# Kernel optimization log

Hardware: AMD Instinct MI355X
Metric: run time of the kernel (lower is better)

The kernel has to match this reference:

```python
import jax, jax.numpy as jnp
import numpy as np

DY = jnp.array([-1, -1, -1, 0, 0, 0, 1, 1, 1], dtype=jnp.float32)
DX = jnp.array([-1, 0, 1, -1, 0, 1, -1, 0, 1], dtype=jnp.float32)
REG = jnp.stack([DY, DX])  # (2,9) regular_matrix: row0 = dy, row1 = dx
EPS = 1e-5


def conv3x3(x, w, b):
    y = jax.lax.conv_general_dilated(x, w, (1, 1), ((1, 1), (1, 1)),
                                     dimension_numbers=('NCHW', 'OIHW', 'NCHW'))
    return y + b[None, :, None, None]


def batchnorm(x, gamma, beta):
    m = x.mean((0, 2, 3), keepdims=True)
    v = x.var((0, 2, 3), keepdims=True)
    return gamma[None, :, None, None] * (x - m) * jax.lax.rsqrt(v + EPS) + beta[None, :, None, None]


def make_offset(tm, tr):
    # tm: (N,4,H,W) per-pixel 2x2 matrix, tr: (N,2,H,W) translation
    N, _, H, W = tm.shape
    M = tm.transpose(0, 2, 3, 1).reshape(N, H, W, 2, 2)
    off = jnp.einsum('nhwij,jk->nhwik', M, REG) - REG          # (N,H,W,2,9)
    off = off.transpose(0, 4, 3, 1, 2)                          # (N,9,2,H,W)
    off = off + tr[:, None, :, :, :]                            # broadcast translation over K
    return off


def deform_conv(x, off, w):
    # x: (N,C,H,W), off: (N,9,2,H,W) with [...,0]=dy,[...,1]=dx, w: (Co,C,3,3)
    N, C, H, W = x.shape
    K = 9
    py = jnp.arange(H, dtype=x.dtype)[None, None, :, None] + DY[None, :, None, None] + off[:, :, 0]
    px = jnp.arange(W, dtype=x.dtype)[None, None, None, :] + DX[None, :, None, None] + off[:, :, 1]
    y0 = jnp.floor(py)
    x0 = jnp.floor(px)
    wy = py - y0
    wx = px - x0
    y0i = y0.astype(jnp.int32)
    x0i = x0.astype(jnp.int32)
    x_flat = x.reshape(N, C, H * W)

    def corner(yi, xi, wgt):
        valid = (yi >= 0) & (yi < H) & (xi >= 0) & (xi < W)
        idx = jnp.clip(yi, 0, H - 1) * W + jnp.clip(xi, 0, W - 1)   # (N,K,H,W)
        g = jax.vmap(lambda xf, ix: xf[:, ix])(x_flat, idx.reshape(N, -1))
        g = g.reshape(N, C, K, H, W)
        return g * (wgt * valid)[:, None]

    cols = (corner(y0i, x0i, (1 - wy) * (1 - wx))
            + corner(y0i, x0i + 1, (1 - wy) * wx)
            + corner(y0i + 1, x0i, wy * (1 - wx))
            + corner(y0i + 1, x0i + 1, wy * wx))
    Co = w.shape[0]
    return jnp.einsum('nckhw,ock->nohw', cols, w.reshape(Co, C, K))


def setup_inputs() -> dict:
    key = jax.random.key(0)
    ks = jax.random.split(key, 16)
    N, C, Co, H, W = 4, 256, 256, 64, 64
    s_off = 0.02   # small init so offsets stay near the regular grid
    s_w = 0.05
    return {
        'x': jax.random.normal(ks[0], (N, C, H, W), jnp.float32),
        'tm1_w': jax.random.normal(ks[1], (4, C, 3, 3), jnp.float32) * s_off,
        'tm1_b': jax.random.normal(ks[2], (4,), jnp.float32) * s_off,
        'tr1_w': jax.random.normal(ks[3], (2, C, 3, 3), jnp.float32) * s_off,
        'tr1_b': jax.random.normal(ks[4], (2,), jnp.float32) * s_off,
        'dcn1_w': jax.random.normal(ks[5], (Co, C, 3, 3), jnp.float32) * s_w,
        'bn1_g': jnp.ones((Co,), jnp.float32),
        'bn1_b': jnp.zeros((Co,), jnp.float32),
        'tm2_w': jax.random.normal(ks[6], (4, Co, 3, 3), jnp.float32) * s_off,
        'tm2_b': jax.random.normal(ks[7], (4,), jnp.float32) * s_off,
        'tr2_w': jax.random.normal(ks[8], (2, Co, 3, 3), jnp.float32) * s_off,
        'tr2_b': jax.random.normal(ks[9], (2,), jnp.float32) * s_off,
        'dcn2_w': jax.random.normal(ks[10], (Co, Co, 3, 3), jnp.float32) * s_w,
        'bn2_g': jnp.ones((Co,), jnp.float32),
        'bn2_b': jnp.zeros((Co,), jnp.float32),
    }


def reference(x, tm1_w, tm1_b, tr1_w, tr1_b, dcn1_w, bn1_g, bn1_b,
              tm2_w, tm2_b, tr2_w, tr2_b, dcn2_w, bn2_g, bn2_b):
    residual = x
    off1 = make_offset(conv3x3(x, tm1_w, tm1_b), conv3x3(x, tr1_w, tr1_b))
    out = deform_conv(x, off1, dcn1_w)
    out = jax.nn.relu(batchnorm(out, bn1_g, bn1_b))
    off2 = make_offset(conv3x3(out, tm2_w, tm2_b), conv3x3(out, tr2_w, tr2_b))
    out = deform_conv(out, off2, dcn2_w)
    out = batchnorm(out, bn2_g, bn2_b)
    return jax.nn.relu(out + residual)
```

## Files before the change

kernel.cpp:

```cpp
#include <hip/hip_runtime.h>
#include <hip/hip_bf16.h>

#define HH 64
#define WW 64
#define HWSZ 4096
#define NBATCH 4
#define CCH 256
#define NPIX 16384
#define CK 2304
#define KSPLIT 3
#define EPSB 1e-5f

typedef __attribute__((ext_vector_type(8))) short bf16x8;
typedef __attribute__((ext_vector_type(4))) float f32x4;

static __device__ __forceinline__ unsigned short f2bf(float f){
  __hip_bfloat16 h = __float2bfloat16(f);
  return *(unsigned short*)&h;
}

__global__ __launch_bounds__(256) void k_transpose_in(const float* __restrict__ x,
                                                      float* __restrict__ xT){
  __shared__ float tile[64][65];
  int hw0 = blockIdx.x * 64;
  int c0  = blockIdx.y * 64;
  int n   = blockIdx.z;
  int t = threadIdx.x;
  int col = t & 63, rb = t >> 6;
#pragma unroll
  for (int r = 0; r < 16; ++r){
    int cl = rb + r*4;
    tile[cl][col] = x[(size_t)(n*CCH + c0 + cl)*HWSZ + hw0 + col];
  }
  __syncthreads();
#pragma unroll
  for (int r = 0; r < 16; ++r){
    int hwl = rb + r*4;
    xT[(size_t)(n*HWSZ + hw0 + hwl)*CCH + c0 + col] = tile[col][hwl];
  }
}

__global__ void k_woff_perm(const float* __restrict__ tmw, const float* __restrict__ trw,
                            float* __restrict__ woff){
  int idx = blockIdx.x*256 + threadIdx.x;
  if (idx >= 9*6*CCH) return;
  int k = idx / (6*CCH); int rem = idx % (6*CCH); int j = rem >> 8; int c = rem & 255;
  float v = (j < 4) ? tmw[(size_t)(j*CCH + c)*9 + k]
                    : trw[(size_t)((j-4)*CCH + c)*9 + k];
  woff[idx] = v;
}

__global__ void k_wgemm_perm(const float* __restrict__ w, __hip_bfloat16* __restrict__ wp){
  int idx = blockIdx.x*256 + threadIdx.x;
  if (idx >= CCH*CK) return;
  int blk = idx >> 13;
  int e   = idx & 8191;
  int o   = e >> 5;
  int el  = e & 31;
  int tap = blk >> 3, cb = blk & 7;
  int c   = cb*32 + (el ^ ((o & 3) << 3));
  wp[idx] = __float2bfloat16(w[(size_t)o*CK + c*9 + tap]);
}

__global__ __launch_bounds__(256) void k_offsets(const float* __restrict__ src,
    const float* __restrict__ wofft, const float* __restrict__ tmb,
    const float* __restrict__ trb, float* __restrict__ off){
  int t = threadIdx.x;
  int wid = t >> 6, lane = t & 63;
  int pbase = blockIdx.x*32 + wid*8;
  int n = pbase >> 12; int hw = pbase & 4095; int h = hw >> 6; int w0 = hw & 63;
  const float* base = src + (size_t)n*HWSZ*CCH + lane*4;

  float acc[8][6];
#pragma unroll
  for (int pi = 0; pi < 8; ++pi)
#pragma unroll
    for (int j = 0; j < 6; ++j) acc[pi][j] = 0.f;

  for (int k = 0; k < 9; ++k){
    int ky = k/3 - 1, kx = k%3 - 1;
    int yy = h + ky;
    if (yy < 0 || yy >= HH) continue;
    float4 wv[6];
#pragma unroll
    for (int j = 0; j < 6; ++j)
      wv[j] = *(const float4*)(wofft + ((k*6 + j) << 8) + lane*4);
#pragma unroll
    for (int pi = 0; pi < 8; ++pi){
      int xx = w0 + pi + kx;
      if (xx < 0 || xx >= WW) continue;
      float4 s4 = *(const float4*)(base + (size_t)(yy*WW + xx)*CCH);
#pragma unroll
      for (int j = 0; j < 6; ++j)
        acc[pi][j] += s4.x*wv[j].x + s4.y*wv[j].y + s4.z*wv[j].z + s4.w*wv[j].w;
    }
  }

#pragma unroll
  for (int pi = 0; pi < 8; ++pi)
#pragma unroll
    for (int j = 0; j < 6; ++j){
      float v = acc[pi][j];
#pragma unroll
      for (int m = 32; m >= 1; m >>= 1) v += __shfl_xor(v, m);
      acc[pi][j] = v;
    }

  float b0 = tmb[0], b1 = tmb[1], b2 = tmb[2], b3 = tmb[3];
  float c0 = trb[0], c1 = trb[1];
  if (lane < 18){
    int k = lane >> 1, comp = lane & 1;
    float dy = (float)(k/3 - 1), dx = (float)(k%3 - 1);
#pragma unroll
    for (int pi = 0; pi < 8; ++pi){
      int p = pbase + pi;
      float val;
      if (comp == 0)
        val = (acc[pi][0] + b0)*dy + (acc[pi][1] + b1)*dx - dy + acc[pi][4] + c0;
      else
        val = (acc[pi][2] + b2)*dy + (acc[pi][3] + b3)*dx - dx + acc[pi][5] + c1;
      off[((size_t)p*9 + k)*2 + comp] = val;
    }
  }
}

__global__ __launch_bounds__(512) void k_dcn(const float* __restrict__ src,
    const float* __restrict__ off, const __hip_bfloat16* __restrict__ wp,
    float* __restrict__ P){
  __shared__ __hip_bfloat16 Al[64*32];
  __shared__ __hip_bfloat16 Bl[256*32];
  __shared__ __align__(16) int   t_off[192][4];
  __shared__ __align__(16) float t_w[192][4];

  int t = threadIdx.x;
  int z = blockIdx.y;
  int pbase = blockIdx.x * 64;

  if (t < 192){
    int px = t / 3, ti = t - px*3;
    int k = z*3 + ti;
    int p = pbase + px;
    int n = p >> 12; int hw = p & 4095; int h = hw >> 6; int w = hw & 63;
    float2 of = *(const float2*)(off + ((size_t)p*9 + k)*2);
    float py = (float)(h + k/3 - 1) + of.x;
    float px_ = (float)(w + (k - (k/3)*3) - 1) + of.y;
    float y0f = floorf(py), x0f = floorf(px_);
    float wy = py - y0f, wx = px_ - x0f;
    int y0 = (int)y0f, x0 = (int)x0f;
    int y1 = y0 + 1, x1 = x0 + 1;
    float w00 = (1.f-wy)*(1.f-wx), w01 = (1.f-wy)*wx;
    float w10 = wy*(1.f-wx),       w11 = wy*wx;
    if (y0 < 0 || y0 >= HH) { w00 = 0.f; w01 = 0.f; }
    if (y1 < 0 || y1 >= HH) { w10 = 0.f; w11 = 0.f; }
    if (x0 < 0 || x0 >= WW) { w00 = 0.f; w10 = 0.f; }
    if (x1 < 0 || x1 >= WW) { w01 = 0.f; w11 = 0.f; }
    int y0c = min(max(y0,0),HH-1), y1c = min(max(y1,0),HH-1);
    int x0c = min(max(x0,0),WW-1), x1c = min(max(x1,0),WW-1);
    int pbix = n << 12;
    t_off[t][0] = (pbix + y0c*WW + x0c) << 10;
    t_off[t][1] = (pbix + y0c*WW + x1c) << 10;
    t_off[t][2] = (pbix + y1c*WW + x0c) << 10;
    t_off[t][3] = (pbix + y1c*WW + x1c) << 10;
    t_w[t][0] = w00; t_w[t][1] = w01; t_w[t][2] = w10; t_w[t][3] = w11;
  }
  __syncthreads();

  int wid = t >> 6, lane = t & 63;
  int pxl = t >> 3, q = t & 7;
  int px3 = pxl * 3, qb = q * 16;
  const char* sbase = (const char*)src;

  int abyte = pxl*64 + ((q*8) ^ ((pxl & 3) << 4));

  int kq = lane >> 4, fr = lane & 15;
  int abr[4], bbr[2];
#pragma unroll
  for (int mi = 0; mi < 4; ++mi){
    int apx = mi*16 + fr;
    abr[mi] = apx*64 + ((kq*16) ^ ((apx & 3) << 4));
  }
#pragma unroll
  for (int ni = 0; ni < 2; ++ni){
    int o = wid*32 + ni*16 + fr;
    bbr[ni] = o*64 + ((kq*16) ^ ((o & 3) << 4));
  }

  f32x4 acc[4][2];
#pragma unroll
  for (int i = 0; i < 4; ++i)
#pragma unroll
    for (int j = 0; j < 2; ++j)
      acc[i][j] = (f32x4){0.f,0.f,0.f,0.f};

  float4 ga, gb, gc, gd, wv;
  {
    int4 o4 = *(const int4*)t_off[px3];
    wv = *(const float4*)t_w[px3];
    ga = *(const float4*)(sbase + (size_t)(unsigned)(o4.x + qb));
    gb = *(const float4*)(sbase + (size_t)(unsigned)(o4.y + qb));
    gc = *(const float4*)(sbase + (size_t)(unsigned)(o4.z + qb));
    gd = *(const float4*)(sbase + (size_t)(unsigned)(o4.w + qb));
  }

  const char* wpz = (const char*)wp + (size_t)(z*24) * 16384;

  for (int kt = 0; kt < 24; ++kt){
    const char* bsrc = wpz + (size_t)kt*16384 + wid*2048 + lane*16;
    char* bdst = (char*)Bl + wid*2048;
#if __has_builtin(__builtin_amdgcn_global_load_lds)
    __builtin_amdgcn_global_load_lds((const __attribute__((address_space(1))) void*)bsrc,
                                     (__attribute__((address_space(3))) void*)bdst, 16, 0, 0);
    __builtin_amdgcn_global_load_lds((const __attribute__((address_space(1))) void*)(bsrc + 1024),
                                     (__attribute__((address_space(3))) void*)(bdst + 1024), 16, 0, 0);
#else
    *(bf16x8*)(bdst + lane*16)        = *(const bf16x8*)bsrc;
    *(bf16x8*)(bdst + 1024 + lane*16) = *(const bf16x8*)(bsrc + 1024);
#endif
    float v0 = wv.x*ga.x + wv.y*gb.x + wv.z*gc.x + wv.w*gd.x;
    float v1 = wv.x*ga.y + wv.y*gb.y + wv.z*gc.y + wv.w*gd.y;
    float v2 = wv.x*ga.z + wv.y*gb.z + wv.z*gc.z + wv.w*gd.z;
    float v3 = wv.x*ga.w + wv.y*gb.w + wv.z*gc.w + wv.w*gd.w;
    ushort4 st;
    st.x = f2bf(v0); st.y = f2bf(v1); st.z = f2bf(v2); st.w = f2bf(v3);

    {
      int ktn = (kt + 1 < 24) ? kt + 1 : 0;
      int slot = px3 + (ktn >> 3);
      int chb = ((ktn & 7) << 7) + qb;
      int4 o4 = *(const int4*)t_off[slot];
      wv = *(const float4*)t_w[slot];
      ga = *(const float4*)(sbase + (size_t)(unsigned)(o4.x + chb));
      gb = *(const float4*)(sbase + (size_t)(unsigned)(o4.y + chb));
      gc = *(const float4*)(sbase + (size_t)(unsigned)(o4.z + chb));
      gd = *(const float4*)(sbase + (size_t)(unsigned)(o4.w + chb));
    }

    *(ushort4*)((char*)Al + abyte) = st;
    __syncthreads();

    bf16x8 av[4], bv[2];
#pragma unroll
    for (int mi = 0; mi < 4; ++mi)
      av[mi] = *(const bf16x8*)((const char*)Al + abr[mi]);
#pragma unroll
    for (int ni = 0; ni < 2; ++ni)
      bv[ni] = *(const bf16x8*)((const char*)Bl + bbr[ni]);
#pragma unroll
    for (int mi = 0; mi < 4; ++mi)
#pragma unroll
      for (int ni = 0; ni < 2; ++ni)
        acc[mi][ni] = __builtin_amdgcn_mfma_f32_16x16x32_bf16(av[mi], bv[ni], acc[mi][ni], 0, 0, 0);
    __syncthreads();
  }

  float* Cp = P + (size_t)z * NPIX * CCH;
#pragma unroll
  for (int mi = 0; mi < 4; ++mi)
#pragma unroll
    for (int ni = 0; ni < 2; ++ni){
      int rr = pbase + mi*16 + (lane>>4)*4;
      int cc = wid*32 + ni*16 + (lane&15);
#pragma unroll
      for (int r = 0; r < 4; ++r)
        Cp[(size_t)(rr + r)*CCH + cc] = acc[mi][ni][r];
    }
}

__global__ __launch_bounds__(256) void k_reduce_stats(const float* __restrict__ P,
    float* __restrict__ v, float* __restrict__ stats){
  int t = threadIdx.x;
  int p0 = blockIdx.x * 64;
  const size_t s1 = (size_t)NPIX * CCH;
  float s = 0.f, ss = 0.f;
#pragma unroll 4
  for (int i = 0; i < 64; ++i){
    size_t idx = (size_t)(p0 + i)*CCH + t;
    float x = P[idx] + P[idx + s1] + P[idx + 2*s1];
    v[idx] = x;
    s += x; ss += x*x;
  }
  atomicAdd(&stats[t], s);
  atomicAdd(&stats[CCH + t], ss);
}

__global__ __launch_bounds__(256) void k_bn_apply(const float* __restrict__ v,
    const float* __restrict__ stats, const float* __restrict__ g,
    const float* __restrict__ bb, float* __restrict__ y){
  const float inv = 1.f/16384.f;
  for (size_t i = (size_t)blockIdx.x*256 + threadIdx.x; i < (size_t)NPIX*CCH;
       i += (size_t)gridDim.x*256){
    int c = (int)(i & 255);
    float mean = stats[c]*inv;
    float var  = stats[CCH + c]*inv - mean*mean;
    float sc = g[c]*rsqrtf(var + EPSB);
    float sh = bb[c] - mean*sc;
    float val = fmaf(v[i], sc, sh);
    y[i] = val > 0.f ? val : 0.f;
  }
}

__global__ __launch_bounds__(256) void k_final(const float* __restrict__ v,
    const float* __restrict__ stats, const float* __restrict__ g,
    const float* __restrict__ bb, const float* __restrict__ x,
    float* __restrict__ out){
  __shared__ float tile[64][65];
  int hw0 = blockIdx.x * 64;
  int o0  = blockIdx.y * 64;
  int n   = blockIdx.z;
  int t = threadIdx.x;
  int col = t & 63, rb = t >> 6;
  const float inv = 1.f/16384.f;
#pragma unroll
  for (int r = 0; r < 16; ++r){
    int pl = rb + r*4;
    tile[pl][col] = v[(size_t)(n*HWSZ + hw0 + pl)*CCH + o0 + col];
  }
  __syncthreads();
#pragma unroll
  for (int r = 0; r < 16; ++r){
    int ol = rb + r*4;
    int o = o0 + ol;
    float mean = stats[o]*inv;
    float var  = stats[CCH + o]*inv - mean*mean;
    float sc = g[o]*rsqrtf(var + EPSB);
    float sh = bb[o] - mean*sc;
    size_t gi = (size_t)(n*CCH + o)*HWSZ + hw0 + col;
    float val = fmaf(tile[col][ol], sc, sh) + x[gi];
    out[gi] = val > 0.f ? val : 0.f;
  }
}

extern "C" void kernel_launch(void* const* d_in, const int* in_sizes, int n_in,
                              void* d_out, int out_size, void* d_ws, size_t ws_size,
                              hipStream_t stream){
  const float* x     = (const float*)d_in[0];
  const float* tm1_w = (const float*)d_in[1];
  const float* tm1_b = (const float*)d_in[2];
  const float* tr1_w = (const float*)d_in[3];
  const float* tr1_b = (const float*)d_in[4];
  const float* dcn1_w= (const float*)d_in[5];
  const float* bn1_g = (const float*)d_in[6];
  const float* bn1_b = (const float*)d_in[7];
  const float* tm2_w = (const float*)d_in[8];
  const float* tm2_b = (const float*)d_in[9];
  const float* tr2_w = (const float*)d_in[10];
  const float* tr2_b = (const float*)d_in[11];
  const float* dcn2_w= (const float*)d_in[12];
  const float* bn2_g = (const float*)d_in[13];
  const float* bn2_b = (const float*)d_in[14];
  float* out = (float*)d_out;

  char* ws = (char*)d_ws;
  size_t cursor = 0;
  auto alloc = [&](size_t bytes)->char*{
    char* p = ws + cursor; cursor += (bytes + 255) & ~(size_t)255; return p;
  };
  float* xT    = (float*)alloc((size_t)NPIX*CCH*4);
  float* ybuf  = (float*)alloc((size_t)NPIX*CCH*4);
  float* gout  = (float*)alloc((size_t)NPIX*CCH*4);
  float* offb  = (float*)alloc((size_t)NPIX*9*2*4);
  float* woff1 = (float*)alloc(9*6*CCH*4);
  float* woff2 = (float*)alloc(9*6*CCH*4);
  __hip_bfloat16* wg1 = (__hip_bfloat16*)alloc((size_t)CCH*CK*2);
  __hip_bfloat16* wg2 = (__hip_bfloat16*)alloc((size_t)CCH*CK*2);
  float* stats = (float*)alloc(1024*4);
  float* pbuf  = (float*)alloc((size_t)KSPLIT*NPIX*CCH*4);

  hipMemsetAsync(stats, 0, 1024*4, stream);
  k_transpose_in<<<dim3(64,4,4),256,0,stream>>>(x, xT);
  k_woff_perm<<<54,256,0,stream>>>(tm1_w, tr1_w, woff1);
  k_woff_perm<<<54,256,0,stream>>>(tm2_w, tr2_w, woff2);
  k_wgemm_perm<<<2304,256,0,stream>>>(dcn1_w, wg1);
  k_wgemm_perm<<<2304,256,0,stream>>>(dcn2_w, wg2);

  k_offsets<<<512,256,0,stream>>>(xT, woff1, tm1_b, tr1_b, offb);
  k_dcn<<<dim3(NPIX/64,KSPLIT),512,0,stream>>>(xT, offb, wg1, pbuf);
  k_reduce_stats<<<NPIX/64,256,0,stream>>>(pbuf, gout, stats);
  k_bn_apply<<<2048,256,0,stream>>>(gout, stats, bn1_g, bn1_b, ybuf);

  k_offsets<<<512,256,0,stream>>>(ybuf, woff2, tm2_b, tr2_b, offb);
  k_dcn<<<dim3(NPIX/64,KSPLIT),512,0,stream>>>(ybuf, offb, wg2, pbuf);
  k_reduce_stats<<<NPIX/64,256,0,stream>>>(pbuf, gout, stats + 512);
  k_final<<<dim3(64,4,4),256,0,stream>>>(gout, stats + 512, bn2_g, bn2_b, x, out);
}
```

Measured before the change: 230.5 us.

## Drop DCN split-K, double-buffer LDS tiles, write GEMM output directly

Removes the 3-way K split in the deformable conv GEMM. Each block now covers all 72 K-tiles, so the kernel writes the final output directly instead of three partial buffers that a reduction kernel had to sum. The main loop double-buffers the A and B tiles in LDS, overlapping the next bilinear gather and weight load with the current MFMAs, and tiles are remapped across blocks with a swizzle. The price is a grid of only 256 blocks of 512 threads, which may underfill the GPU, plus more LDS per block.

After: 219.3 us. 1.05x faster.

```diff
diff --git a/kernel.cpp b/kernel.cpp
--- a/kernel.cpp
+++ b/kernel.cpp
@@ -8,7 +8,6 @@
 #define CCH 256
 #define NPIX 16384
 #define CK 2304
-#define KSPLIT 3
 #define EPSB 1e-5f
 
 typedef __attribute__((ext_vector_type(8))) short bf16x8;
@@ -18,6 +17,13 @@
   __hip_bfloat16 h = __float2bfloat16(f);
   return *(unsigned short*)&h;
 }
+
+#if __has_builtin(__builtin_amdgcn_global_load_lds)
+#define GLD(S,D) __builtin_amdgcn_global_load_lds((const __attribute__((address_space(1))) void*)(S), \
+                                                  (__attribute__((address_space(3))) void*)(D), 16, 0, 0)
+#else
+#define GLD(S,D) (*(bf16x8*)((char*)(D) + lane*16) = *(const bf16x8*)(S))
+#endif
 
 __global__ __launch_bounds__(256) void k_transpose_in(const float* __restrict__ x,
                                                       float* __restrict__ xT){
@@ -126,19 +132,19 @@
 
 __global__ __launch_bounds__(512) void k_dcn(const float* __restrict__ src,
     const float* __restrict__ off, const __hip_bfloat16* __restrict__ wp,
-    float* __restrict__ P){
-  __shared__ __hip_bfloat16 Al[64*32];
-  __shared__ __hip_bfloat16 Bl[256*32];
-  __shared__ __align__(16) int   t_off[192][4];
-  __shared__ __align__(16) float t_w[192][4];
-
-  int t = threadIdx.x;
-  int z = blockIdx.y;
-  int pbase = blockIdx.x * 64;
-
-  if (t < 192){
-    int px = t / 3, ti = t - px*3;
-    int k = z*3 + ti;
+    float* __restrict__ gout){
+  __shared__ __hip_bfloat16 Al[2*64*32];
+  __shared__ __hip_bfloat16 Bl[2*256*32];
+  __shared__ __align__(16) int   t_off[576][4];
+  __shared__ __align__(16) float t_w[576][4];
+
+  int t = threadIdx.x;
+  int bid = blockIdx.x;
+  int tile = (bid & 7)*32 + (bid >> 3);
+  int pbase = tile * 64;
+
+  for (int s = t; s < 576; s += 512){
+    int px = s / 9, k = s - px*9;
     int p = pbase + px;
     int n = p >> 12; int hw = p & 4095; int h = hw >> 6; int w = hw & 63;
     float2 of = *(const float2*)(off + ((size_t)p*9 + k)*2);
@@ -157,18 +163,18 @@
     int y0c = min(max(y0,0),HH-1), y1c = min(max(y1,0),HH-1);
     int x0c = min(max(x0,0),WW-1), x1c = min(max(x1,0),WW-1);
     int pbix = n << 12;
-    t_off[t][0] = (pbix + y0c*WW + x0c) << 10;
-    t_off[t][1] = (pbix + y0c*WW + x1c) << 10;
-    t_off[t][2] = (pbix + y1c*WW + x0c) << 10;
-    t_off[t][3] = (pbix + y1c*WW + x1c) << 10;
-    t_w[t][0] = w00; t_w[t][1] = w01; t_w[t][2] = w10; t_w[t][3] = w11;
+    t_off[s][0] = (pbix + y0c*WW + x0c) << 10;
+    t_off[s][1] = (pbix + y0c*WW + x1c) << 10;
+    t_off[s][2] = (pbix + y1c*WW + x0c) << 10;
+    t_off[s][3] = (pbix + y1c*WW + x1c) << 10;
+    t_w[s][0] = w00; t_w[s][1] = w01; t_w[s][2] = w10; t_w[s][3] = w11;
   }
   __syncthreads();
 
   int wid = t >> 6, lane = t & 63;
   int pxl = t >> 3, q = t & 7;
-  int px3 = pxl * 3, qb = q * 16;
   const char* sbase = (const char*)src;
+  const char* wpb = (const char*)wp;
 
   int abyte = pxl*64 + ((q*8) ^ ((pxl & 3) << 4));
 
@@ -192,91 +198,88 @@
     for (int j = 0; j < 2; ++j)
       acc[i][j] = (f32x4){0.f,0.f,0.f,0.f};
 
-  float4 ga, gb, gc, gd, wv;
   {
-    int4 o4 = *(const int4*)t_off[px3];
-    wv = *(const float4*)t_w[px3];
-    ga = *(const float4*)(sbase + (size_t)(unsigned)(o4.x + qb));
-    gb = *(const float4*)(sbase + (size_t)(unsigned)(o4.y + qb));
-    gc = *(const float4*)(sbase + (size_t)(unsigned)(o4.z + qb));
-    gd = *(const float4*)(sbase + (size_t)(unsigned)(o4.w + qb));
-  }
-
-  const char* wpz = (const char*)wp + (size_t)(z*24) * 16384;
-
-  for (int kt = 0; kt < 24; ++kt){
-    const char* bsrc = wpz + (size_t)kt*16384 + wid*2048 + lane*16;
-    char* bdst = (char*)Bl + wid*2048;
-#if __has_builtin(__builtin_amdgcn_global_load_lds)
-    __builtin_amdgcn_global_load_lds((const __attribute__((address_space(1))) void*)bsrc,
-                                     (__attribute__((address_space(3))) void*)bdst, 16, 0, 0);
-    __builtin_amdgcn_global_load_lds((const __attribute__((address_space(1))) void*)(bsrc + 1024),
-                                     (__attribute__((address_space(3))) void*)(bdst + 1024), 16, 0, 0);
-#else
-    *(bf16x8*)(bdst + lane*16)        = *(const bf16x8*)bsrc;
-    *(bf16x8*)(bdst + 1024 + lane*16) = *(const bf16x8*)(bsrc + 1024);
-#endif
+    int slot = pxl*9;
+    int chb = q << 4;
+    int4 o4 = *(const int4*)t_off[slot];
+    float4 wv = *(const float4*)t_w[slot];
+    float4 ga = *(const float4*)(sbase + (size_t)(unsigned)(o4.x + chb));
+    float4 gb = *(const float4*)(sbase + (size_t)(unsigned)(o4.y + chb));
+    float4 gc = *(const float4*)(sbase + (size_t)(unsigned)(o4.z + chb));
+    float4 gd = *(const float4*)(sbase + (size_t)(unsigned)(o4.w + chb));
+    const char* bsrc = wpb + wid*2048 + lane*16;
+    GLD(bsrc,        (char*)Bl + wid*2048);
+    GLD(bsrc + 1024, (char*)Bl + wid*2048 + 1024);
     float v0 = wv.x*ga.x + wv.y*gb.x + wv.z*gc.x + wv.w*gd.x;
     float v1 = wv.x*ga.y + wv.y*gb.y + wv.z*gc.y + wv.w*gd.y;
     float v2 = wv.x*ga.z + wv.y*gb.z + wv.z*gc.z + wv.w*gd.z;
     float v3 = wv.x*ga.w + wv.y*gb.w + wv.z*gc.w + wv.w*gd.w;
-    ushort4 st;
-    st.x = f2bf(v0); st.y = f2bf(v1); st.z = f2bf(v2); st.w = f2bf(v3);
-
-    {
-      int ktn = (kt + 1 < 24) ? kt + 1 : 0;
-      int slot = px3 + (ktn >> 3);
-      int chb = ((ktn & 7) << 7) + qb;
-      int4 o4 = *(const int4*)t_off[slot];
-      wv = *(const float4*)t_w[slot];
-      ga = *(const float4*)(sbase + (size_t)(unsigned)(o4.x + chb));
-      gb = *(const float4*)(sbase + (size_t)(unsigned)(o4.y + chb));
-      gc = *(const float4*)(sbase + (size_t)(unsigned)(o4.z + chb));
-      gd = *(const float4*)(sbase + (size_t)(unsigned)(o4.w + chb));
-    }
-
+    ushort4 st; st.x = f2bf(v0); st.y = f2bf(v1); st.z = f2bf(v2); st.w = f2bf(v3);
     *(ushort4*)((char*)Al + abyte) = st;
     __syncthreads();
-
-    bf16x8 av[4], bv[2];
-#pragma unroll
-    for (int mi = 0; mi < 4; ++mi)
-      av[mi] = *(const bf16x8*)((const char*)Al + abr[mi]);
-#pragma unroll
-    for (int ni = 0; ni < 2; ++ni)
-      bv[ni] = *(const bf16x8*)((const char*)Bl + bbr[ni]);
-#pragma unroll
-    for (int mi = 0; mi < 4; ++mi)
-#pragma unroll
-      for (int ni = 0; ni < 2; ++ni)
-        acc[mi][ni] = __builtin_amdgcn_mfma_f32_16x16x32_bf16(av[mi], bv[ni], acc[mi][ni], 0, 0, 0);
+  }
+
+  for (int kt = 0; kt < 72; ++kt){
+    int cur = kt & 1, nxt = cur ^ 1;
+    int ktn = (kt < 71) ? kt + 1 : 71;
+    int slotn = pxl*9 + (ktn >> 3);
+    int chb = ((ktn & 7) << 7) + (q << 4);
+    int4 o4 = *(const int4*)t_off[slotn];
+    float4 wv = *(const float4*)t_w[slotn];
+    float4 ga = *(const float4*)(sbase + (size_t)(unsigned)(o4.x + chb));
+    float4 gb = *(const float4*)(sbase + (size_t)(unsigned)(o4.y + chb));
+    float4 gc = *(const float4*)(sbase + (size_t)(unsigned)(o4.z + chb));
+    float4 gd = *(const float4*)(sbase + (size_t)(unsigned)(o4.w + chb));
+    const char* bsrc = wpb + (size_t)ktn*16384 + wid*2048 + lane*16;
+    char* bdst = (char*)Bl + nxt*16384 + wid*2048;
+    GLD(bsrc,        bdst);
+    GLD(bsrc + 1024, bdst + 1024);
+
+    const char* Ac = (const char*)Al + cur*4096;
+    const char* Bc = (const char*)Bl + cur*16384;
+    bf16x8 av0 = *(const bf16x8*)(Ac + abr[0]);
+    bf16x8 av1 = *(const bf16x8*)(Ac + abr[1]);
+    bf16x8 av2 = *(const bf16x8*)(Ac + abr[2]);
+    bf16x8 av3 = *(const bf16x8*)(Ac + abr[3]);
+    bf16x8 bv0 = *(const bf16x8*)(Bc + bbr[0]);
+    bf16x8 bv1 = *(const bf16x8*)(Bc + bbr[1]);
+    acc[0][0] = __builtin_amdgcn_mfma_f32_16x16x32_bf16(av0, bv0, acc[0][0], 0, 0, 0);
+    acc[0][1] = __builtin_amdgcn_mfma_f32_16x16x32_bf16(av0, bv1, acc[0][1], 0, 0, 0);
+    acc[1][0] = __builtin_amdgcn_mfma_f32_16x16x32_bf16(av1, bv0, acc[1][0], 0, 0, 0);
+    acc[1][1] = __builtin_amdgcn_mfma_f32_16x16x32_bf16(av1, bv1, acc[1][1], 0, 0, 0);
+    acc[2][0] = __builtin_amdgcn_mfma_f32_16x16x32_bf16(av2, bv0, acc[2][0], 0, 0, 0);
+    acc[2][1] = __builtin_amdgcn_mfma_f32_16x16x32_bf16(av2, bv1, acc[2][1], 0, 0, 0);
+    acc[3][0] = __builtin_amdgcn_mfma_f32_16x16x32_bf16(av3, bv0, acc[3][0], 0, 0, 0);
+    acc[3][1] = __builtin_amdgcn_mfma_f32_16x16x32_bf16(av3, bv1, acc[3][1], 0, 0, 0);
+
+    float v0 = wv.x*ga.x + wv.y*gb.x + wv.z*gc.x + wv.w*gd.x;
+    float v1 = wv.x*ga.y + wv.y*gb.y + wv.z*gc.y + wv.w*gd.y;
+    float v2 = wv.x*ga.z + wv.y*gb.z + wv.z*gc.z + wv.w*gd.z;
+    float v3 = wv.x*ga.w + wv.y*gb.w + wv.z*gc.w + wv.w*gd.w;
+    ushort4 st; st.x = f2bf(v0); st.y = f2bf(v1); st.z = f2bf(v2); st.w = f2bf(v3);
+    *(ushort4*)((char*)Al + nxt*4096 + abyte) = st;
     __syncthreads();
   }
 
-  float* Cp = P + (size_t)z * NPIX * CCH;
 #pragma unroll
   for (int mi = 0; mi < 4; ++mi)
 #pragma unroll
     for (int ni = 0; ni < 2; ++ni){
       int rr = pbase + mi*16 + (lane>>4)*4;
-      int cc = wid*32 + ni*16 + (lane&15);
+      int cc = wid*32 + ni*16 + fr;
 #pragma unroll
       for (int r = 0; r < 4; ++r)
-        Cp[(size_t)(rr + r)*CCH + cc] = acc[mi][ni][r];
+        gout[(size_t)(rr + r)*CCH + cc] = acc[mi][ni][r];
     }
 }
 
-__global__ __launch_bounds__(256) void k_reduce_stats(const float* __restrict__ P,
-    float* __restrict__ v, float* __restrict__ stats){
-  int t = threadIdx.x;
-  int p0 = blockIdx.x * 64;
-  const size_t s1 = (size_t)NPIX * CCH;
+__global__ __launch_bounds__(256) void k_bn_stats(const float* __restrict__ v,
+                                                  float* __restrict__ stats){
+  int t = threadIdx.x;
+  int p0 = blockIdx.x * 128;
   float s = 0.f, ss = 0.f;
-#pragma unroll 4
-  for (int i = 0; i < 64; ++i){
-    size_t idx = (size_t)(p0 + i)*CCH + t;
-    float x = P[idx] + P[idx + s1] + P[idx + 2*s1];
-    v[idx] = x;
+  for (int i = 0; i < 128; ++i){
+    float x = v[(size_t)(p0 + i)*CCH + t];
     s += x; ss += x*x;
   }
   atomicAdd(&stats[t], s);
@@ -364,7 +367,6 @@
   __hip_bfloat16* wg1 = (__hip_bfloat16*)alloc((size_t)CCH*CK*2);
   __hip_bfloat16* wg2 = (__hip_bfloat16*)alloc((size_t)CCH*CK*2);
   float* stats = (float*)alloc(1024*4);
-  float* pbuf  = (float*)alloc((size_t)KSPLIT*NPIX*CCH*4);
 
   hipMemsetAsync(stats, 0, 1024*4, stream);
   k_transpose_in<<<dim3(64,4,4),256,0,stream>>>(x, xT);
@@ -374,12 +376,12 @@
   k_wgemm_perm<<<2304,256,0,stream>>>(dcn2_w, wg2);
 
   k_offsets<<<512,256,0,stream>>>(xT, woff1, tm1_b, tr1_b, offb);
-  k_dcn<<<dim3(NPIX/64,KSPLIT),512,0,stream>>>(xT, offb, wg1, pbuf);
-  k_reduce_stats<<<NPIX/64,256,0,stream>>>(pbuf, gout, stats);
+  k_dcn<<<256,512,0,stream>>>(xT, offb, wg1, gout);
+  k_bn_stats<<<128,256,0,stream>>>(gout, stats);
   k_bn_apply<<<2048,256,0,stream>>>(gout, stats, bn1_g, bn1_b, ybuf);
 
   k_offsets<<<512,256,0,stream>>>(ybuf, woff2, tm2_b, tr2_b, offb);
-  k_dcn<<<dim3(NPIX/64,KSPLIT),512,0,stream>>>(ybuf, offb, wg2, pbuf);
-  k_reduce_stats<<<NPIX/64,256,0,stream>>>(pbuf, gout, stats + 512);
+  k_dcn<<<256,512,0,stream>>>(ybuf, offb, wg2, gout);
+  k_bn_stats<<<128,256,0,stream>>>(gout, stats + 512);
   k_final<<<dim3(64,4,4),256,0,stream>>>(gout, stats + 512, bn2_g, bn2_b, x, out);
 }
```
